# Kernel optimization log

Measured on AMD Instinct MI355X. Metric: run time of the kernel, lower is better.

## Reference

```python
import jax, jax.numpy as jnp
import numpy as np

N = 2048      # nodes
E = 65536     # edges (avg degree 32)
D_I = 64      # input feature dim
D_O = 64      # output feature dim
EPS = 1e-6


def _one_hot_incidence(key, n, e):
    # each edge column has a single 1 at its endpoint node row -> [N, E]
    idx = jax.random.randint(key, (e,), 0, n)
    return jnp.zeros((n, e), jnp.float32).at[idx, jnp.arange(e)].set(1.0)


def setup_inputs() -> dict:
    key = jax.random.key(0)
    k_x, k_s, k_t, k_wf, k_ww = jax.random.split(key, 5)
    x = jax.random.normal(k_x, (N, D_I), jnp.float32)
    src = _one_hot_incidence(k_s, N, E)
    tgt = _one_hot_incidence(k_t, N, E)
    # xavier-uniform init for Linear(2*d_i, d_o) and Linear(2*d_i, 1)
    lim_f = float(np.sqrt(6.0 / (2 * D_I + D_O)))
    lim_w = float(np.sqrt(6.0 / (2 * D_I + 1)))
    W_f = jax.random.uniform(k_wf, (2 * D_I, D_O), jnp.float32, -lim_f, lim_f)
    b_f = jnp.zeros((D_O,), jnp.float32)
    W_w = jax.random.uniform(k_ww, (2 * D_I, 1), jnp.float32, -lim_w, lim_w)
    b_w = jnp.zeros((1,), jnp.float32)
    return {"x": x, "src": src, "tgt": tgt,
            "W_f": W_f, "b_f": b_f, "W_w": W_w, "b_w": b_w}


def reference(x, src, tgt, W_f, b_f, W_w, b_w):
    # gather source/target node features per edge via dense one-hot matmuls
    hsrc = src.T @ x                      # [E, d_i]
    htgt = tgt.T @ x                      # [E, d_i]
    h = jnp.concatenate([hsrc, htgt], axis=1)   # [E, 2*d_i]
    y = jax.nn.relu(h @ W_f + b_f)        # [E, d_o]
    a = h @ W_w + b_w                     # [E, 1]
    a_max = jnp.mean(a, axis=0, keepdims=True)
    a_exp = jnp.exp(a - a_max)            # [E, 1]
    a_sum = tgt @ a_exp                   # [N, 1] segment-sum over edges per target node
    a_tgt = tgt.T @ a_sum                 # [E, 1] broadcast denominators back to edges
    a_att = a_exp / (a_tgt + EPS)         # edge softmax weights
    o = tgt @ (y * a_att)                 # [N, d_o] weighted scatter-sum
    return o
```

## Files before the change

kernel.cpp:

```cpp
#include <hip/hip_runtime.h>
#include <hip/hip_bf16.h>

#define N_NODES 2048
#define N_EDGES 65536
#define D_IN    64
#define D_OUT   64
#define GAT_EPS 1e-6f

typedef unsigned short u16;
typedef unsigned int   u32;
typedef __attribute__((ext_vector_type(8))) short frag8;
typedef __attribute__((ext_vector_type(4))) float f32x4;

__device__ __forceinline__ u16 f2bf(float f) {
    union { u32 u; float f; } x; x.f = f;
    u32 lsb = (x.u >> 16) & 1u;
    x.u += 0x7fffu + lsb;
    return (u16)(x.u >> 16);
}

__global__ void k_extract(const uint4* __restrict__ src, const uint4* __restrict__ tgt,
                          int* __restrict__ sidx, int* __restrict__ tidx,
                          float* __restrict__ zero_base) {
    u32 b = blockIdx.x, tid = threadIdx.x;
    if (b < 520u) {
        u32 zi = b * 256u + tid;
        if (zi < 133120u) zero_base[zi] = 0.0f;
    }
    const uint4* m; int* idx;
    if (b < 2048u) { m = src; idx = sidx; }
    else           { m = tgt; idx = tidx; b -= 2048u; }
    u32 t0 = b * 256u + tid;
    const u32 S = 524288u;
    #pragma unroll 4
    for (u32 it = 0; it < 64u; ++it) {
        u32 t = t0 + it * S;
        uint4 v = m[t];
        if (v.x | v.y | v.z | v.w) {
            u32 elem = t * 4u;
            int n = (int)(elem >> 16);
            int e = (int)(elem & 65535u);
            if (v.x) idx[e]     = n;
            if (v.y) idx[e + 1] = n;
            if (v.z) idx[e + 2] = n;
            if (v.w) idx[e + 3] = n;
        }
    }
}

__global__ void __launch_bounds__(256) k_fused(
        const float* __restrict__ x,
        const int* __restrict__ sidx, const int* __restrict__ tidx,
        const float* __restrict__ Wf, const float* __restrict__ bf,
        const float* __restrict__ Ww, const float* __restrict__ bw,
        float* __restrict__ a_sum, float* __restrict__ out_acc) {
    __shared__ u16 wt[D_OUT * 2 * D_IN];
    __shared__ float ww[2 * D_IN];
    int tid = threadIdx.x;
    if (tid < 2 * D_IN) ww[tid] = Ww[tid];
    for (int i = tid; i < 2 * D_IN * D_OUT; i += 256) {
        int k = i >> 6, d = i & 63;
        wt[d * 128 + k] = f2bf(Wf[i]);
    }
    __syncthreads();

    int wave = tid >> 6, lane = tid & 63;
    int q = lane >> 4, r = lane & 15;
    int e0 = blockIdx.x * 64 + wave * 16;

    int s_r = sidx[e0 + r] & (N_NODES - 1);
    int t_r = tidx[e0 + r] & (N_NODES - 1);
    const float* xs = x + s_r * D_IN;
    const float* xt = x + t_r * D_IN;

    frag8 afr[4];
    float part = 0.0f;
    #pragma unroll
    for (int c = 0; c < 4; ++c) {
        const float* base = (c < 2 ? xs : xt) + (c & 1) * 32 + q * 8;
        int kb = (c >> 1) * 64 + (c & 1) * 32 + q * 8;
        float4 lo = *(const float4*)(base);
        float4 hi = *(const float4*)(base + 4);
        part += lo.x * ww[kb]     + lo.y * ww[kb + 1]
              + lo.z * ww[kb + 2] + lo.w * ww[kb + 3]
              + hi.x * ww[kb + 4] + hi.y * ww[kb + 5]
              + hi.z * ww[kb + 6] + hi.w * ww[kb + 7];
        frag8 f;
        f[0] = (short)f2bf(lo.x); f[1] = (short)f2bf(lo.y);
        f[2] = (short)f2bf(lo.z); f[3] = (short)f2bf(lo.w);
        f[4] = (short)f2bf(hi.x); f[5] = (short)f2bf(hi.y);
        f[6] = (short)f2bf(hi.z); f[7] = (short)f2bf(hi.w);
        afr[c] = f;
    }
    part += __shfl_xor(part, 16);
    part += __shfl_xor(part, 32);
    float ae = expf(part + bw[0]);
    if (lane < 16) atomicAdd(&a_sum[t_r], ae);

    f32x4 acc[4] = { {0,0,0,0}, {0,0,0,0}, {0,0,0,0}, {0,0,0,0} };
    #pragma unroll
    for (int c = 0; c < 4; ++c) {
        #pragma unroll
        for (int dt = 0; dt < 4; ++dt) {
            frag8 bfr = *(const frag8*)(&wt[(dt * 16 + r) * 128 + c * 32 + q * 8]);
            acc[dt] = __builtin_amdgcn_mfma_f32_16x16x32_bf16(afr[c], bfr, acc[dt], 0, 0, 0);
        }
    }

    #pragma unroll
    for (int reg = 0; reg < 4; ++reg) {
        float w  = __shfl(ae,  q * 4 + reg);
        int   tg = __shfl(t_r, q * 4 + reg);
        #pragma unroll
        for (int dt = 0; dt < 4; ++dt) {
            int d = dt * 16 + r;
            float y = acc[dt][reg] + bf[d];
            y = y > 0.0f ? y : 0.0f;
            atomicAdd(&out_acc[tg * D_OUT + d], y * w);
        }
    }
}

__global__ void k_norm(const float* __restrict__ out_acc, const float* __restrict__ a_sum,
                       float* __restrict__ out) {
    int i = blockIdx.x * 256 + threadIdx.x;
    out[i] = out_acc[i] / (a_sum[i >> 6] + GAT_EPS);
}

extern "C" void kernel_launch(void* const* d_in, const int* in_sizes, int n_in,
                              void* d_out, int out_size, void* d_ws, size_t ws_size,
                              hipStream_t stream) {
    const float* x   = (const float*)d_in[0];
    const float* src = (const float*)d_in[1];
    const float* tgt = (const float*)d_in[2];
    const float* Wf  = (const float*)d_in[3];
    const float* bf  = (const float*)d_in[4];
    const float* Ww  = (const float*)d_in[5];
    const float* bw  = (const float*)d_in[6];
    float* out = (float*)d_out;

    char* ws = (char*)d_ws;
    float* a_sum   = (float*)(ws);
    float* out_acc = (float*)(ws + 8192);
    int*   sidx    = (int*)  (ws + 8192 + 524288);
    int*   tidx    = (int*)  (ws + 532480 + 262144);

    k_extract<<<4096, 256, 0, stream>>>((const uint4*)src, (const uint4*)tgt,
                                        sidx, tidx, (float*)ws);
    k_fused<<<N_EDGES / 64, 256, 0, stream>>>(x, sidx, tidx, Wf, bf, Ww, bw,
                                              a_sum, out_acc);
    k_norm<<<(N_NODES * D_OUT) / 256, 256, 0, stream>>>(out_acc, a_sum, out);
}
```

Before: 992.0 us.

## Precompute per-node projections and aggregate edges via CSR instead of atomics

After: 997.7 us. About the same (+0.6%).

```diff
diff --git a/kernel.cpp b/kernel.cpp
--- a/kernel.cpp
+++ b/kernel.cpp
@@ -1,36 +1,54 @@
 #include <hip/hip_runtime.h>
-#include <hip/hip_bf16.h>
 
 #define N_NODES 2048
 #define N_EDGES 65536
-#define D_IN    64
-#define D_OUT   64
+#define D       64
 #define GAT_EPS 1e-6f
 
-typedef unsigned short u16;
-typedef unsigned int   u32;
-typedef __attribute__((ext_vector_type(8))) short frag8;
-typedef __attribute__((ext_vector_type(4))) float f32x4;
+typedef unsigned int u32;
 
-__device__ __forceinline__ u16 f2bf(float f) {
-    union { u32 u; float f; } x; x.f = f;
-    u32 lsb = (x.u >> 16) & 1u;
-    x.u += 0x7fffu + lsb;
-    return (u16)(x.u >> 16);
-}
-
-__global__ void k_extract(const uint4* __restrict__ src, const uint4* __restrict__ tgt,
-                          int* __restrict__ sidx, int* __restrict__ tidx,
-                          float* __restrict__ zero_base) {
+__global__ void __launch_bounds__(256) k_front(
+        const uint4* __restrict__ src, const uint4* __restrict__ tgt,
+        const float* __restrict__ x,
+        const float* __restrict__ Wf, const float* __restrict__ bf,
+        const float* __restrict__ Ww, const float* __restrict__ bw,
+        float* __restrict__ P, float* __restrict__ Qb,
+        float* __restrict__ u, float* __restrict__ vb,
+        int* __restrict__ cnt,
+        int* __restrict__ sidx, int* __restrict__ tidx) {
     u32 b = blockIdx.x, tid = threadIdx.x;
+    if (b < 512u) {
+        u32 i = b * 256u + tid;
+        u32 n = i >> 6, d = i & 63u;
+        const float* xr = x + n * 64u;
+        float accP = 0.f, accQ = bf[d];
+        #pragma unroll
+        for (int k = 0; k < 64; ++k) {
+            float xv = xr[k];
+            accP = fmaf(xv, Wf[k * 64 + d], accP);
+            accQ = fmaf(xv, Wf[(k + 64) * 64 + d], accQ);
+        }
+        P[i] = accP; Qb[i] = accQ;
+        return;
+    }
     if (b < 520u) {
-        u32 zi = b * 256u + tid;
-        if (zi < 133120u) zero_base[zi] = 0.0f;
+        u32 n = (b - 512u) * 256u + tid;
+        const float* xr = x + n * 64u;
+        float au = 0.f, av = bw[0];
+        #pragma unroll
+        for (int k = 0; k < 64; ++k) {
+            float xv = xr[k];
+            au = fmaf(xv, Ww[k], au);
+            av = fmaf(xv, Ww[64 + k], av);
+        }
+        u[n] = au; vb[n] = av; cnt[n] = 0;
+        return;
     }
+    u32 eb = b - 520u;
     const uint4* m; int* idx;
-    if (b < 2048u) { m = src; idx = sidx; }
-    else           { m = tgt; idx = tidx; b -= 2048u; }
-    u32 t0 = b * 256u + tid;
+    if (eb < 2048u) { m = src; idx = sidx; }
+    else            { m = tgt; idx = tidx; eb -= 2048u; }
+    u32 t0 = eb * 256u + tid;
     const u32 S = 524288u;
     #pragma unroll 4
     for (u32 it = 0; it < 64u; ++it) {
@@ -48,83 +66,93 @@
     }
 }
 
-__global__ void __launch_bounds__(256) k_fused(
-        const float* __restrict__ x,
-        const int* __restrict__ sidx, const int* __restrict__ tidx,
-        const float* __restrict__ Wf, const float* __restrict__ bf,
-        const float* __restrict__ Ww, const float* __restrict__ bw,
-        float* __restrict__ a_sum, float* __restrict__ out_acc) {
-    __shared__ u16 wt[D_OUT * 2 * D_IN];
-    __shared__ float ww[2 * D_IN];
-    int tid = threadIdx.x;
-    if (tid < 2 * D_IN) ww[tid] = Ww[tid];
-    for (int i = tid; i < 2 * D_IN * D_OUT; i += 256) {
-        int k = i >> 6, d = i & 63;
-        wt[d * 128 + k] = f2bf(Wf[i]);
+__global__ void __launch_bounds__(256) k_count(const int* __restrict__ tidx,
+                                               int* __restrict__ cnt) {
+    int e = blockIdx.x * 256 + threadIdx.x;
+    atomicAdd(&cnt[tidx[e] & (N_NODES - 1)], 1);
+}
+
+__global__ void __launch_bounds__(256) k_scan(const int* __restrict__ cnt,
+                                              int* __restrict__ row_start,
+                                              int* __restrict__ cursor) {
+    __shared__ int part[256];
+    int t = threadIdx.x;
+    int c[8]; int s = 0;
+    #pragma unroll
+    for (int j = 0; j < 8; ++j) { c[j] = cnt[t * 8 + j]; s += c[j]; }
+    part[t] = s;
+    __syncthreads();
+    for (int off = 1; off < 256; off <<= 1) {
+        int v = (t >= off) ? part[t - off] : 0;
+        __syncthreads();
+        part[t] += v;
+        __syncthreads();
     }
-    __syncthreads();
+    int base = (t == 0) ? 0 : part[t - 1];
+    #pragma unroll
+    for (int j = 0; j < 8; ++j) {
+        row_start[t * 8 + j] = base;
+        cursor[t * 8 + j]    = base;
+        base += c[j];
+    }
+    if (t == 255) row_start[2048] = base;
+}
 
-    int wave = tid >> 6, lane = tid & 63;
-    int q = lane >> 4, r = lane & 15;
-    int e0 = blockIdx.x * 64 + wave * 16;
+__global__ void __launch_bounds__(256) k_bucket(const int* __restrict__ tidx,
+                                                int* __restrict__ cursor,
+                                                int* __restrict__ csr) {
+    int e = blockIdx.x * 256 + threadIdx.x;
+    int t = tidx[e] & (N_NODES - 1);
+    int p = atomicAdd(&cursor[t], 1);
+    csr[p & (N_EDGES - 1)] = e;
+}
 
-    int s_r = sidx[e0 + r] & (N_NODES - 1);
-    int t_r = tidx[e0 + r] & (N_NODES - 1);
-    const float* xs = x + s_r * D_IN;
-    const float* xt = x + t_r * D_IN;
-
-    frag8 afr[4];
-    float part = 0.0f;
-    #pragma unroll
-    for (int c = 0; c < 4; ++c) {
-        const float* base = (c < 2 ? xs : xt) + (c & 1) * 32 + q * 8;
-        int kb = (c >> 1) * 64 + (c & 1) * 32 + q * 8;
-        float4 lo = *(const float4*)(base);
-        float4 hi = *(const float4*)(base + 4);
-        part += lo.x * ww[kb]     + lo.y * ww[kb + 1]
-              + lo.z * ww[kb + 2] + lo.w * ww[kb + 3]
-              + hi.x * ww[kb + 4] + hi.y * ww[kb + 5]
-              + hi.z * ww[kb + 6] + hi.w * ww[kb + 7];
-        frag8 f;
-        f[0] = (short)f2bf(lo.x); f[1] = (short)f2bf(lo.y);
-        f[2] = (short)f2bf(lo.z); f[3] = (short)f2bf(lo.w);
-        f[4] = (short)f2bf(hi.x); f[5] = (short)f2bf(hi.y);
-        f[6] = (short)f2bf(hi.z); f[7] = (short)f2bf(hi.w);
-        afr[c] = f;
-    }
-    part += __shfl_xor(part, 16);
-    part += __shfl_xor(part, 32);
-    float ae = expf(part + bw[0]);
-    if (lane < 16) atomicAdd(&a_sum[t_r], ae);
-
-    f32x4 acc[4] = { {0,0,0,0}, {0,0,0,0}, {0,0,0,0}, {0,0,0,0} };
-    #pragma unroll
-    for (int c = 0; c < 4; ++c) {
-        #pragma unroll
-        for (int dt = 0; dt < 4; ++dt) {
-            frag8 bfr = *(const frag8*)(&wt[(dt * 16 + r) * 128 + c * 32 + q * 8]);
-            acc[dt] = __builtin_amdgcn_mfma_f32_16x16x32_bf16(afr[c], bfr, acc[dt], 0, 0, 0);
+__global__ void __launch_bounds__(256) k_out(
+        const float* __restrict__ P, const float* __restrict__ Qb,
+        const float* __restrict__ u, const float* __restrict__ vb,
+        const int* __restrict__ sidx, const int* __restrict__ row_start,
+        const int* __restrict__ csr, float* __restrict__ out) {
+    int tid  = threadIdx.x;
+    int lane = tid & 63;
+    int n    = blockIdx.x * 4 + (tid >> 6);
+    int start = row_start[n], end = row_start[n + 1];
+    float qd = Qb[n * 64 + lane];
+    float vn = vb[n];
+    float acc = 0.f, asum = 0.f;
+    for (int base = start; base < end; base += 64) {
+        int m = end - base;
+        float a_l = 0.f; int s_l = 0;
+        if (lane < m) {
+            int e = csr[base + lane] & (N_EDGES - 1);
+            s_l = sidx[e] & (N_NODES - 1);
+            a_l = __expf(u[s_l] + vn);
+        }
+        int c = m < 64 ? m : 64;
+        int j = 0;
+        for (; j + 4 <= c; j += 4) {
+            int   s0 = __shfl(s_l, j),     s1 = __shfl(s_l, j + 1);
+            int   s2 = __shfl(s_l, j + 2), s3 = __shfl(s_l, j + 3);
+            float a0 = __shfl(a_l, j),     a1 = __shfl(a_l, j + 1);
+            float a2 = __shfl(a_l, j + 2), a3 = __shfl(a_l, j + 3);
+            float y0 = P[s0 * 64 + lane] + qd;
+            float y1 = P[s1 * 64 + lane] + qd;
+            float y2 = P[s2 * 64 + lane] + qd;
+            float y3 = P[s3 * 64 + lane] + qd;
+            asum += (a0 + a1) + (a2 + a3);
+            acc = fmaf(a0, fmaxf(y0, 0.f), acc);
+            acc = fmaf(a1, fmaxf(y1, 0.f), acc);
+            acc = fmaf(a2, fmaxf(y2, 0.f), acc);
+            acc = fmaf(a3, fmaxf(y3, 0.f), acc);
+        }
+        for (; j < c; ++j) {
+            int   s = __shfl(s_l, j);
+            float a = __shfl(a_l, j);
+            float y = P[s * 64 + lane] + qd;
+            asum += a;
+            acc = fmaf(a, fmaxf(y, 0.f), acc);
         }
     }
-
-    #pragma unroll
-    for (int reg = 0; reg < 4; ++reg) {
-        float w  = __shfl(ae,  q * 4 + reg);
-        int   tg = __shfl(t_r, q * 4 + reg);
-        #pragma unroll
-        for (int dt = 0; dt < 4; ++dt) {
-            int d = dt * 16 + r;
-            float y = acc[dt][reg] + bf[d];
-            y = y > 0.0f ? y : 0.0f;
-            atomicAdd(&out_acc[tg * D_OUT + d], y * w);
-        }
-    }
-}
-
-__global__ void k_norm(const float* __restrict__ out_acc, const float* __restrict__ a_sum,
-                       float* __restrict__ out) {
-    int i = blockIdx.x * 256 + threadIdx.x;
-    out[i] = out_acc[i] / (a_sum[i >> 6] + GAT_EPS);
+    out[n * 64 + lane] = acc / (asum + GAT_EPS);
 }
 
 extern "C" void kernel_launch(void* const* d_in, const int* in_sizes, int n_in,
@@ -140,14 +168,22 @@
     float* out = (float*)d_out;
 
     char* ws = (char*)d_ws;
-    float* a_sum   = (float*)(ws);
-    float* out_acc = (float*)(ws + 8192);
-    int*   sidx    = (int*)  (ws + 8192 + 524288);
-    int*   tidx    = (int*)  (ws + 532480 + 262144);
+    float* P     = (float*)(ws);
+    float* Qb    = (float*)(ws + 524288);
+    float* u     = (float*)(ws + 1048576);
+    float* vb    = (float*)(ws + 1056768);
+    int*   cnt   = (int*)  (ws + 1064960);
+    int*   row_s = (int*)  (ws + 1073152);
+    int*   curs  = (int*)  (ws + 1081600);
+    int*   sidx  = (int*)  (ws + 1089792);
+    int*   tidx  = (int*)  (ws + 1351936);
+    int*   csr   = (int*)  (ws + 1614080);
 
-    k_extract<<<4096, 256, 0, stream>>>((const uint4*)src, (const uint4*)tgt,
-                                        sidx, tidx, (float*)ws);
-    k_fused<<<N_EDGES / 64, 256, 0, stream>>>(x, sidx, tidx, Wf, bf, Ww, bw,
-                                              a_sum, out_acc);
-    k_norm<<<(N_NODES * D_OUT) / 256, 256, 0, stream>>>(out_acc, a_sum, out);
+    k_front<<<4616, 256, 0, stream>>>((const uint4*)src, (const uint4*)tgt, x,
+                                      Wf, bf, Ww, bw, P, Qb, u, vb, cnt,
+                                      sidx, tidx);
+    k_count<<<N_EDGES / 256, 256, 0, stream>>>(tidx, cnt);
+    k_scan<<<1, 256, 0, stream>>>(cnt, row_s, curs);
+    k_bucket<<<N_EDGES / 256, 256, 0, stream>>>(tidx, curs, csr);
+    k_out<<<N_NODES / 4, 256, 0, stream>>>(P, Qb, u, vb, sidx, row_s, csr, out);
 }
```
